# Performance work log

Hardware: AMD Instinct MI355X
Metric: run time of the kernel (lower is better)

## Reference

```python
import jax, jax.numpy as jnp
import numpy as np

NUM_CLASS = 4
EMB_SIZE = 2048
S = 16.0


def setup_inputs() -> dict:
    key = jax.random.key(0)
    k1, k2, k3 = jax.random.split(key, 3)
    fea = jax.random.normal(k1, (16384, EMB_SIZE), dtype=jnp.float32)
    # nn.Linear default init: U(-1/sqrt(fan_in), 1/sqrt(fan_in))
    bound = 1.0 / np.sqrt(EMB_SIZE)
    W = jax.random.uniform(k2, (NUM_CLASS, EMB_SIZE), dtype=jnp.float32, minval=-bound, maxval=bound)
    b = jax.random.uniform(k3, (NUM_CLASS,), dtype=jnp.float32, minval=-bound, maxval=bound)
    return {"fea": fea, "W": W, "b": b}


def reference(fea, W, b):
    # L2 normalize along axis=1 (torch.norm(p=2, dim=1, keepdim=True); no eps)
    norm = jnp.sqrt(jnp.sum(fea * fea, axis=1, keepdims=True))  # [B, 1]
    fea_n = fea / norm
    # Linear: y = x @ W^T + b, then scalar scale
    logit = (jnp.einsum('be,ce->bc', fea_n, W) + b) * S  # [B, num_class]
    return logit
```

## Files before the change

kernel.cpp:

```cpp
#include <hip/hip_runtime.h>

#define EMB 2048
#define NC 4
#define NROWS 16384
#define SCALE_S 16.0f

#define ROWS_PER_WAVE 4
#define WAVES_PER_BLOCK 4
#define ROWS_PER_BLOCK (ROWS_PER_WAVE * WAVES_PER_BLOCK)

__global__ __launch_bounds__(256) void binary_head_kernel(
    const float* __restrict__ fea,
    const float* __restrict__ W,
    const float* __restrict__ bias,
    float* __restrict__ out)
{
    __shared__ float4 sW[NC * (EMB / 4)];

    const int tid = threadIdx.x;

    const float4* W4 = (const float4*)W;
#pragma unroll
    for (int i = 0; i < 8; ++i) {
        sW[i * 256 + tid] = W4[i * 256 + tid];
    }
    __syncthreads();

    const int wave = tid >> 6;
    const int lane = tid & 63;

    const float bval = bias[lane & (NC - 1)];

    const float4* fea4 = (const float4*)fea;
    const int rowBase = blockIdx.x * ROWS_PER_BLOCK + wave * ROWS_PER_WAVE;

    for (int r = 0; r < ROWS_PER_WAVE; ++r) {
        const int row = rowBase + r;
        const float4* frow = fea4 + (size_t)row * (EMB / 4);

        float4 x[8];
#pragma unroll
        for (int j = 0; j < 8; ++j) {
            x[j] = frow[j * 64 + lane];
        }

        float ss = 0.0f, d0 = 0.0f, d1 = 0.0f, d2 = 0.0f, d3 = 0.0f;
#pragma unroll
        for (int j = 0; j < 8; ++j) {
            const float4 v = x[j];
            const int col = j * 64 + lane;

            ss += v.x * v.x + v.y * v.y + v.z * v.z + v.w * v.w;

            const float4 w0 = sW[0 * 512 + col];
            d0 += v.x * w0.x + v.y * w0.y + v.z * w0.z + v.w * w0.w;
            const float4 w1 = sW[1 * 512 + col];
            d1 += v.x * w1.x + v.y * w1.y + v.z * w1.z + v.w * w1.w;
            const float4 w2 = sW[2 * 512 + col];
            d2 += v.x * w2.x + v.y * w2.y + v.z * w2.z + v.w * w2.w;
            const float4 w3 = sW[3 * 512 + col];
            d3 += v.x * w3.x + v.y * w3.y + v.z * w3.z + v.w * w3.w;
        }

#pragma unroll
        for (int m = 1; m < 64; m <<= 1) {
            ss += __shfl_xor(ss, m, 64);
            d0 += __shfl_xor(d0, m, 64);
            d1 += __shfl_xor(d1, m, 64);
            d2 += __shfl_xor(d2, m, 64);
            d3 += __shfl_xor(d3, m, 64);
        }

        if (lane < NC) {
            const float d = (lane == 0) ? d0 : (lane == 1) ? d1 : (lane == 2) ? d2 : d3;
            const float inv = rsqrtf(ss);
            out[row * NC + lane] = (d * inv + bval) * SCALE_S;
        }
    }
}

extern "C" void kernel_launch(void* const* d_in, const int* in_sizes, int n_in,
                              void* d_out, int out_size, void* d_ws, size_t ws_size,
                              hipStream_t stream) {
    const float* fea  = (const float*)d_in[0];
    const float* W    = (const float*)d_in[1];
    const float* bias = (const float*)d_in[2];
    float* out = (float*)d_out;

    const int grid = NROWS / ROWS_PER_BLOCK;
    binary_head_kernel<<<grid, 256, 0, stream>>>(fea, W, bias, out);
}
```

Before: 191.3 us.

## Keep weights in registers and double-buffer row loads across iterations

Each lane now loads its slice of the weight matrix into registers instead of staging it in shared memory, which removes the LDS traffic and the block barrier. Each wave handles 8 rows instead of 4 and prefetches the next row's features into a second register buffer while the current row is computed. The goal is more loads in flight for this bandwidth-bound read of fea. The cost is much higher register pressure (about 64 extra VGPRs for weights plus two feature buffers), which may limit occupancy, and the last row is loaded redundantly because of the clamp.

```diff
diff --git a/kernel.cpp b/kernel.cpp
--- a/kernel.cpp
+++ b/kernel.cpp
@@ -5,61 +5,61 @@
 #define NROWS 16384
 #define SCALE_S 16.0f
 
-#define ROWS_PER_WAVE 4
+#define ROWS_PER_WAVE 8
 #define WAVES_PER_BLOCK 4
-#define ROWS_PER_BLOCK (ROWS_PER_WAVE * WAVES_PER_BLOCK)
 
-__global__ __launch_bounds__(256) void binary_head_kernel(
+__global__ __launch_bounds__(256, 2) void binary_head_kernel(
     const float* __restrict__ fea,
     const float* __restrict__ W,
     const float* __restrict__ bias,
     float* __restrict__ out)
 {
-    __shared__ float4 sW[NC * (EMB / 4)];
-
-    const int tid = threadIdx.x;
-
-    const float4* W4 = (const float4*)W;
-#pragma unroll
-    for (int i = 0; i < 8; ++i) {
-        sW[i * 256 + tid] = W4[i * 256 + tid];
-    }
-    __syncthreads();
-
+    const int tid  = threadIdx.x;
     const int wave = tid >> 6;
     const int lane = tid & 63;
 
+    const float4* W4 = (const float4*)W;
+    float4 w[NC][8];
+#pragma unroll
+    for (int c = 0; c < NC; ++c) {
+#pragma unroll
+        for (int j = 0; j < 8; ++j) {
+            w[c][j] = W4[c * (EMB / 4) + j * 64 + lane];
+        }
+    }
+
     const float bval = bias[lane & (NC - 1)];
 
+    const int gwave = blockIdx.x * WAVES_PER_BLOCK + wave;
+    const int row0  = gwave * ROWS_PER_WAVE;
     const float4* fea4 = (const float4*)fea;
-    const int rowBase = blockIdx.x * ROWS_PER_BLOCK + wave * ROWS_PER_WAVE;
 
+    float4 xa[8], xb[8];
+    {
+        const float4* frow = fea4 + (size_t)row0 * (EMB / 4);
+#pragma unroll
+        for (int j = 0; j < 8; ++j) xa[j] = frow[j * 64 + lane];
+    }
+
+#pragma unroll
     for (int r = 0; r < ROWS_PER_WAVE; ++r) {
-        const int row = rowBase + r;
-        const float4* frow = fea4 + (size_t)row * (EMB / 4);
-
-        float4 x[8];
+        {
+            int pr = row0 + r + 1;
+            if (pr > NROWS - 1) pr = NROWS - 1;
+            const float4* fn = fea4 + (size_t)pr * (EMB / 4);
 #pragma unroll
-        for (int j = 0; j < 8; ++j) {
-            x[j] = frow[j * 64 + lane];
+            for (int j = 0; j < 8; ++j) xb[j] = fn[j * 64 + lane];
         }
 
         float ss = 0.0f, d0 = 0.0f, d1 = 0.0f, d2 = 0.0f, d3 = 0.0f;
 #pragma unroll
         for (int j = 0; j < 8; ++j) {
-            const float4 v = x[j];
-            const int col = j * 64 + lane;
-
+            const float4 v = xa[j];
             ss += v.x * v.x + v.y * v.y + v.z * v.z + v.w * v.w;
-
-            const float4 w0 = sW[0 * 512 + col];
-            d0 += v.x * w0.x + v.y * w0.y + v.z * w0.z + v.w * w0.w;
-            const float4 w1 = sW[1 * 512 + col];
-            d1 += v.x * w1.x + v.y * w1.y + v.z * w1.z + v.w * w1.w;
-            const float4 w2 = sW[2 * 512 + col];
-            d2 += v.x * w2.x + v.y * w2.y + v.z * w2.z + v.w * w2.w;
-            const float4 w3 = sW[3 * 512 + col];
-            d3 += v.x * w3.x + v.y * w3.y + v.z * w3.z + v.w * w3.w;
+            d0 += v.x * w[0][j].x + v.y * w[0][j].y + v.z * w[0][j].z + v.w * w[0][j].w;
+            d1 += v.x * w[1][j].x + v.y * w[1][j].y + v.z * w[1][j].z + v.w * w[1][j].w;
+            d2 += v.x * w[2][j].x + v.y * w[2][j].y + v.z * w[2][j].z + v.w * w[2][j].w;
+            d3 += v.x * w[3][j].x + v.y * w[3][j].y + v.z * w[3][j].z + v.w * w[3][j].w;
         }
 
 #pragma unroll
@@ -73,9 +73,11 @@
 
         if (lane < NC) {
             const float d = (lane == 0) ? d0 : (lane == 1) ? d1 : (lane == 2) ? d2 : d3;
-            const float inv = rsqrtf(ss);
-            out[row * NC + lane] = (d * inv + bval) * SCALE_S;
+            out[(row0 + r) * NC + lane] = (d * rsqrtf(ss) + bval) * SCALE_S;
         }
+
+#pragma unroll
+        for (int j = 0; j < 8; ++j) xa[j] = xb[j];
     }
 }
 
@@ -87,6 +89,6 @@
     const float* bias = (const float*)d_in[2];
     float* out = (float*)d_out;
 
-    const int grid = NROWS / ROWS_PER_BLOCK;
+    const int grid = NROWS / (ROWS_PER_WAVE * WAVES_PER_BLOCK);
     binary_head_kernel<<<grid, 256, 0, stream>>>(fea, W, bias, out);
 }
```

Result: no change. 193.0 us (+0.9%).
